# Performance work log

Hardware: AMD Instinct MI355X
Metric: run time of the kernel (lower is better)

## Reference

```python
import jax, jax.numpy as jnp
import numpy as np

# Config matching init_kwargs / module defaults
B_T2I, B_LM, B_MMU = 2, 2, 2
B = B_T2I + B_LM + B_MMU
S = 1280
H, D = 16, 64
IMAGE_BE = [(128, 1152)]          # t2i_image_begin_end
MMU_END = 1027
PAD_BE = [(0, 80), (0, 100), (0, 110), (0, 0)]  # create_block_mask default pad_begin_ends


def _mixed_mask():
    """Vectorized translation of OmniAttentionMechanism.mixed_mask -> bool [B,S,S]."""
    q = jnp.arange(S)[:, None]    # [S,1] query index
    kv = jnp.arange(S)[None, :]   # [1,S] key index

    # t2i_full_begin / t2i_full_end (per-q image block bounds)
    full_begin = jnp.arange(S)
    full_end = jnp.arange(S)
    for ib, ie in IMAGE_BE:
        full_begin = full_begin.at[ib:ie].set(ib)
        full_end = full_end.at[ib:ie].set(ie)

    # pad_ends[b, kv]: arange baseline, first len(PAD_BE) batches get pad region end
    pad_ends = jnp.tile(jnp.arange(S)[None, :], (B, 1))
    for cnt, (pb, pe) in enumerate(PAD_BE):
        pad_ends = pad_ends.at[cnt, pb:pe].set(pe)

    # t2i: padded-causal OR bidirectional image block
    causal = (~(kv < pad_ends[:, None, :]) & (q >= kv)) | (q == kv)   # [B,S,S]
    full = (kv < full_end[:, None]) & (kv >= full_begin[:, None])     # [S,S] (q-indexed bounds)
    t2i = causal | full[None]
    lm = (q >= kv)[None]                                              # [1,S,S]
    mmu = ((q >= kv) | (kv < MMU_END))[None]                          # [1,S,S]

    b = jnp.arange(B)[:, None, None]
    # Faithful to the original XOR composition (terms are batch-disjoint so == OR)
    return ((b < B_T2I) & t2i) ^ ((b >= B_T2I) & (b < B_T2I + B_LM) & lm) ^ ((b >= B_T2I + B_LM) & mmu)


def setup_inputs() -> dict:
    key = jax.random.key(0)
    kq, kk, kv = jax.random.split(key, 3)
    shape = (B, H, S, D)
    return {
        "q": jax.random.normal(kq, shape, dtype=jnp.float32),
        "k": jax.random.normal(kk, shape, dtype=jnp.float32),
        "v": jax.random.normal(kv, shape, dtype=jnp.float32),
    }


def reference(q, k, v):
    """flex_attention(q, k, v, block_mask=mixed-t2i-lm-mmu) equivalent."""
    mask = _mixed_mask()[:, None]  # [B,1,S,S], broadcast over heads
    scale = 1.0 / jnp.sqrt(jnp.float32(D))  # flex_attention default scale
    scores = jnp.einsum('bhqd,bhkd->bhqk', q, k) * scale
    scores = jnp.where(mask, scores, -jnp.inf)  # every row has >=1 allowed key (q==kv / q>=kv)
    attn = jax.nn.softmax(scores, axis=-1)
    return jnp.einsum('bhqk,bhkd->bhqd', attn, v)
```

## Files before the change

kernel.cpp:

```cpp
#include <hip/hip_runtime.h>
#include <hip/hip_bf16.h>
#include <math.h>


#define SS 1280
#define DD 64
#define NH 16
#define TK 64
#define QB 128
#define NITEMS 960

typedef __attribute__((ext_vector_type(8))) short bf16x8;
typedef __attribute__((ext_vector_type(16))) float f32x16;

union UA { uint u[4]; bf16x8 v; };

__device__ inline uint pk2(float a, float b) {
    union { __hip_bfloat162 h; uint u; } cv;
    cv.h = __float22bfloat162_rn(float2{a, b});
    return cv.u;
}

__device__ inline void pl32(uint& a, uint& b) {
    asm volatile("v_permlane32_swap_b32 %0, %1" : "+v"(a), "+v"(b));
}

#define WAITVM2() asm volatile("s_waitcnt vmcnt(2)" ::: "memory")

__device__ inline void decode_item(int i, int& b, int& h, int& qt) {
    if (i < 96)  { qt = 9; b = i / 16; h = i % 16; return; }
    i -= 96;
    if (i < 256) { b = i / 128; qt = 1 + (i % 128) / 16; h = i % 16; return; }
    i -= 256;
    if (i < 32)  { b = 2 + i / 16; qt = 8; h = i % 16; return; }
    i -= 32;
    if (i < 32)  { b = 4 + i / 16; qt = 8; h = i % 16; return; }
    i -= 32;
    if (i < 256) { b = 4 + i / 128; qt = (i % 128) / 16; h = i % 16; return; }
    i -= 256;
    if (i < 224) { qt = 7 - i / 32; b = 2 + (i % 32) / 16; h = i % 16; return; }
    i -= 224;
    if (i < 32)  { b = 2 + i / 16; qt = 0; h = i % 16; return; }
    i -= 32;
    b = i / 16; qt = 0; h = i % 16;
}

__global__ __launch_bounds__(256) void prepass8(
    const float* __restrict__ K, const float* __restrict__ V,
    ushort* __restrict__ Kb, ushort* __restrict__ Vtb)
{
    const int gx = blockIdx.x;
    const int t  = threadIdx.x;
    if (gx < 3840) {
        const size_t e = ((size_t)gx * 256 + t) * 8;
        const float4 a = *(const float4*)(K + e);
        const float4 c = *(const float4*)(K + e + 4);
        UA u;
        u.u[0] = pk2(a.x, a.y); u.u[1] = pk2(a.z, a.w);
        u.u[2] = pk2(c.x, c.y); u.u[3] = pk2(c.z, c.w);
        *(bf16x8*)(Kb + e) = u.v;
    } else {
        const int g   = gx - 3840;
        const int kvt = g % 20;
        const int p   = g / 20;
        __shared__ float T[64 * 67];
#pragma unroll
        for (int i = 0; i < 16; ++i) {
            const int idx = t + 256 * i;
            T[(idx >> 6) * 67 + (idx & 63)] = V[(size_t)p * (SS * DD) + (size_t)(kvt * 64) * DD + idx];
        }
        __syncthreads();
        ushort* dst = Vtb + (size_t)p * (DD * SS) + kvt * 64;
#pragma unroll
        for (int i = 0; i < 2; ++i) {
            const int c0 = t + 256 * i;
            const int d = c0 >> 3, kc = c0 & 7;
            UA u;
#pragma unroll
            for (int j = 0; j < 4; ++j)
                u.u[j] = pk2(T[(kc * 8 + 2 * j) * 67 + d], T[(kc * 8 + 2 * j + 1) * 67 + d]);
            *(bf16x8*)(dst + (size_t)d * SS + kc * 8) = u.v;
        }
    }
}

__global__ __launch_bounds__(256) void omni_attn15(
    const float* __restrict__ Q, const ushort* __restrict__ Kb,
    const ushort* __restrict__ Vtb, float* __restrict__ O)
{
    int b, h, qt;
    decode_item(blockIdx.x, b, h, qt);

    const int t   = threadIdx.x;
    const int w   = t >> 6;
    const int l   = t & 63;
    const int l31 = l & 31;
    const int hi2 = l >> 5;

    const int p   = b * NH + h;
    const int qb0 = qt * QB;
    const int qw0 = qb0 + w * 32;
    const int qr  = qw0 + l31;
    const size_t pbase = (size_t)p * (SS * DD);

    const int bt = (b < 2) ? 0 : (b < 4) ? 1 : 2;
    const int pe = (b == 0) ? 80 : (b == 1) ? 100 : 0;
    const int qmax_blk = qb0 + QB - 1;
    const int qmax_w   = qw0 + 31;
    const bool blk_img = (qb0 + QB - 1 >= 128) && (qb0 < 1152);
    const bool w_img   = (qw0 >= 128) && (qw0 < 1152);

    __shared__ char smem[3 * 8192];

    const float scale = 0.125f * 1.44269504088896340736f;

    int koff[2];
#pragma unroll
    for (int rd = 0; rd < 2; ++rd) {
        const int ci  = rd * 256 + w * 64 + l;
        const int row = ci >> 3, cc = ci & 7;
        koff[rd] = row * DD + (cc ^ (row & 7)) * 8;
    }

    bf16x8 qf[4];
#pragma unroll
    for (int ks = 0; ks < 4; ++ks) {
        const float* src = Q + pbase + (size_t)qr * DD + ks * 16 + hi2 * 8;
        const float4 a = *(const float4*)(src);
        const float4 c = *(const float4*)(src + 4);
        UA u;
        u.u[0] = pk2(a.x * scale, a.y * scale); u.u[1] = pk2(a.z * scale, a.w * scale);
        u.u[2] = pk2(c.x * scale, c.y * scale); u.u[3] = pk2(c.z * scale, c.w * scale);
        qf[ks] = u.v;
    }

    f32x16 o_acc[2];
#pragma unroll
    for (int ntd = 0; ntd < 2; ++ntd)
#pragma unroll
        for (int r = 0; r < 16; ++r) o_acc[ntd][r] = 0.f;
    float psum = 0.f;

    auto need_blk = [&](int k0) -> bool {
        if (bt == 0) return (k0 <= qmax_blk) || (blk_img && k0 >= 128 && k0 < 1152);
        if (bt == 1) return (k0 <= qmax_blk);
        return (k0 <= qmax_blk) || (k0 < 1027);
    };
    auto next_tile = [&](int k) -> int {
        k += TK;
        while (k < SS && !need_blk(k)) k += TK;
        return k;
    };
    auto stageK = [&](int bsel, int k0s) {
        char* buf = smem + bsel * 8192;
        const ushort* Kp = Kb + pbase + (size_t)k0s * DD;
#pragma unroll
        for (int rd = 0; rd < 2; ++rd) {
            char* lb = buf + (rd * 256 + w * 64) * 16;
            __builtin_amdgcn_global_load_lds(
                (const __attribute__((address_space(1))) void*)(Kp + koff[rd]),
                (__attribute__((address_space(3))) void*)lb, 16, 0, 0);
        }
    };

    const ushort* vrow0 = Vtb + pbase + (size_t)l31 * SS + hi2 * 8;
    const ushort* vrow1 = vrow0 + 32 * SS;

    int ka = 0, cur = 0;
    int kb = next_tile(0);
    int kc = (kb < SS) ? next_tile(kb) : SS;
    stageK(0, ka);
    stageK(1, kb);
    WAITVM2();
    __builtin_amdgcn_s_barrier();
    __builtin_amdgcn_sched_barrier(0);

    while (true) {
        const int k0 = ka;
        const bool kv_img = (k0 >= 128) && (k0 < 1152);
        bool need_w, full_w;
        if (bt == 0) {
            need_w = (k0 <= qmax_w) || (w_img && kv_img);
            full_w = ((k0 >= pe) && (k0 + 63 <= qw0)) || (w_img && kv_img);
        } else if (bt == 1) {
            need_w = (k0 <= qmax_w);
            full_w = (k0 + 63 <= qw0);
        } else {
            need_w = (k0 <= qmax_w) || (k0 < 1027);
            full_w = (k0 + 63 <= qw0) || (k0 + 63 < 1027);
        }

        if (need_w) {
            char* cbuf = smem + cur * 8192;
#pragma unroll
            for (int nt = 0; nt < 2; ++nt) {
                const int vb = k0 + nt * 32;
                bf16x8 vfn[4];
                vfn[0] = *(const bf16x8*)(vrow0 + vb);
                vfn[1] = *(const bf16x8*)(vrow0 + vb + 16);
                vfn[2] = *(const bf16x8*)(vrow1 + vb);
                vfn[3] = *(const bf16x8*)(vrow1 + vb + 16);

                f32x16 s;
#pragma unroll
                for (int r = 0; r < 16; ++r) s[r] = 0.f;
                __builtin_amdgcn_s_setprio(1);
#pragma unroll
                for (int ksd = 0; ksd < 4; ++ksd) {
                    const int row = nt * 32 + l31;
                    int off = row * 128 + ksd * 32 + hi2 * 16;
                    off ^= (row & 7) << 4;
                    const bf16x8 kf = *(const bf16x8*)(cbuf + off);
                    s = __builtin_amdgcn_mfma_f32_32x32x16_bf16(kf, qf[ksd], s, 0, 0, 0);
                }
                __builtin_amdgcn_s_setprio(0);

                const int c0k = k0 + nt * 32;
                uint c[8];
#pragma unroll
                for (int i = 0; i < 8; ++i) {
                    float pa, pb;
                    if (full_w) {
                        pa = __builtin_amdgcn_exp2f(s[2 * i]);
                        pb = __builtin_amdgcn_exp2f(s[2 * i + 1]);
                    } else {
                        const int r0i = 2 * i, r1i = 2 * i + 1;
                        const int kva = c0k + (r0i & 3) + 8 * (r0i >> 2) + 4 * hi2;
                        const int kvb = c0k + (r1i & 3) + 8 * (r1i >> 2) + 4 * hi2;
                        bool aa, ab;
                        if (bt == 0) {
                            aa = (qr == kva) | ((kva >= pe) & (qr >= kva)) |
                                 ((qr >= 128) & (qr < 1152) & (kva >= 128) & (kva < 1152));
                            ab = (qr == kvb) | ((kvb >= pe) & (qr >= kvb)) |
                                 ((qr >= 128) & (qr < 1152) & (kvb >= 128) & (kvb < 1152));
                        } else if (bt == 1) {
                            aa = (qr >= kva); ab = (qr >= kvb);
                        } else {
                            aa = (qr >= kva) | (kva < 1027);
                            ab = (qr >= kvb) | (kvb < 1027);
                        }
                        pa = aa ? __builtin_amdgcn_exp2f(s[2 * i]) : 0.f;
                        pb = ab ? __builtin_amdgcn_exp2f(s[2 * i + 1]) : 0.f;
                    }
                    psum += pa + pb;
                    c[i] = pk2(pa, pb);
                }

                UA A0, A1;
                {
                    uint a0 = c[0], b0 = c[2]; pl32(a0, b0);
                    uint a1 = c[1], b1 = c[3]; pl32(a1, b1);
                    A0.u[0] = a0; A0.u[1] = a1; A0.u[2] = b0; A0.u[3] = b1;
                    uint a2 = c[4], b2 = c[6]; pl32(a2, b2);
                    uint a3 = c[5], b3 = c[7]; pl32(a3, b3);
                    A1.u[0] = a2; A1.u[1] = a3; A1.u[2] = b2; A1.u[3] = b3;
                }

                __builtin_amdgcn_s_setprio(1);
                o_acc[0] = __builtin_amdgcn_mfma_f32_32x32x16_bf16(A0.v, vfn[0], o_acc[0], 0, 0, 0);
                o_acc[0] = __builtin_amdgcn_mfma_f32_32x32x16_bf16(A1.v, vfn[1], o_acc[0], 0, 0, 0);
                o_acc[1] = __builtin_amdgcn_mfma_f32_32x32x16_bf16(A0.v, vfn[2], o_acc[1], 0, 0, 0);
                o_acc[1] = __builtin_amdgcn_mfma_f32_32x32x16_bf16(A1.v, vfn[3], o_acc[1], 0, 0, 0);
                __builtin_amdgcn_s_setprio(0);
            }
        }

        stageK((cur + 2) % 3, (kc < SS) ? kc : 0);
        WAITVM2();
        __builtin_amdgcn_s_barrier();
        __builtin_amdgcn_sched_barrier(0);
        if (kb >= SS) break;
        ka = kb; kb = kc; kc = (kc < SS) ? next_tile(kc) : SS;
        cur = (cur + 1) % 3;
    }

    psum += __shfl_xor(psum, 32, 64);
#pragma unroll
    for (int r = 0; r < 16; ++r) {
        const int q_loc = (r & 3) + 8 * (r >> 2) + 4 * hi2;
        const float tv = __shfl(psum, q_loc, 64);
        const float iv = 1.f / tv;
        float* dst = O + pbase + (size_t)(qw0 + q_loc) * DD + l31;
#pragma unroll
        for (int ntd = 0; ntd < 2; ++ntd)
            dst[ntd * 32] = o_acc[ntd][r] * iv;
    }
}

extern "C" void kernel_launch(void* const* d_in, const int* in_sizes, int n_in,
                              void* d_out, int out_size, void* d_ws, size_t ws_size,
                              hipStream_t stream) {
    const float* q = (const float*)d_in[0];
    const float* k = (const float*)d_in[1];
    const float* v = (const float*)d_in[2];
    float* o = (float*)d_out;

    const size_t NE = 7864320ULL;
    ushort* Kb  = (ushort*)d_ws;
    ushort* Vtb = Kb + NE;

    prepass8<<<dim3(5760), 256, 0, stream>>>(k, v, Kb, Vtb);
    omni_attn15<<<dim3(NITEMS), 256, 0, stream>>>(q, Kb, Vtb, o);
}
```

Before: 100.6 us.

## Load K fragments directly from global memory, drop LDS staging pipeline

Replaces the triple-buffered LDS staging of K tiles (global_load_lds plus per-tile barriers) with direct per-wave global loads of K fragments into registers. Tile skipping becomes per-wave instead of per-block, so waves iterate independently without workgroup synchronisation. This removes barrier stalls and LDS traffic, but gives up explicit prefetch and makes the four waves each fetch the same K rows from cache, which may expose global load latency.

```diff
diff --git a/kernel.cpp b/kernel.cpp
--- a/kernel.cpp
+++ b/kernel.cpp
@@ -24,8 +24,6 @@
 __device__ inline void pl32(uint& a, uint& b) {
     asm volatile("v_permlane32_swap_b32 %0, %1" : "+v"(a), "+v"(b));
 }
-
-#define WAITVM2() asm volatile("s_waitcnt vmcnt(2)" ::: "memory")
 
 __device__ inline void decode_item(int i, int& b, int& h, int& qt) {
     if (i < 96)  { qt = 9; b = i / 16; h = i % 16; return; }
@@ -84,7 +82,7 @@
     }
 }
 
-__global__ __launch_bounds__(256) void omni_attn15(
+__global__ __launch_bounds__(256) void omni_attn16(
     const float* __restrict__ Q, const ushort* __restrict__ Kb,
     const ushort* __restrict__ Vtb, float* __restrict__ O)
 {
@@ -105,22 +103,10 @@
 
     const int bt = (b < 2) ? 0 : (b < 4) ? 1 : 2;
     const int pe = (b == 0) ? 80 : (b == 1) ? 100 : 0;
-    const int qmax_blk = qb0 + QB - 1;
-    const int qmax_w   = qw0 + 31;
-    const bool blk_img = (qb0 + QB - 1 >= 128) && (qb0 < 1152);
-    const bool w_img   = (qw0 >= 128) && (qw0 < 1152);
-
-    __shared__ char smem[3 * 8192];
+    const int qmax_w = qw0 + 31;
+    const bool w_img = (qw0 >= 128) && (qw0 < 1152);
 
     const float scale = 0.125f * 1.44269504088896340736f;
-
-    int koff[2];
-#pragma unroll
-    for (int rd = 0; rd < 2; ++rd) {
-        const int ci  = rd * 256 + w * 64 + l;
-        const int row = ci >> 3, cc = ci & 7;
-        koff[rd] = row * DD + (cc ^ (row & 7)) * 8;
-    }
 
     bf16x8 qf[4];
 #pragma unroll
@@ -141,137 +127,97 @@
         for (int r = 0; r < 16; ++r) o_acc[ntd][r] = 0.f;
     float psum = 0.f;
 
-    auto need_blk = [&](int k0) -> bool {
-        if (bt == 0) return (k0 <= qmax_blk) || (blk_img && k0 >= 128 && k0 < 1152);
-        if (bt == 1) return (k0 <= qmax_blk);
-        return (k0 <= qmax_blk) || (k0 < 1027);
+    const ushort* kfb = Kb + pbase + (size_t)l31 * DD + hi2 * 8;
+    const ushort* vr0 = Vtb + pbase + (size_t)l31 * SS + hi2 * 8;
+    const ushort* vr1 = vr0 + 32 * SS;
+
+    auto need_w_f = [&](int k0) -> bool {
+        if (bt == 0) return (k0 <= qmax_w) || (w_img && k0 >= 128 && k0 < 1152);
+        if (bt == 1) return (k0 <= qmax_w);
+        return (k0 <= qmax_w) || (k0 < 1027);
     };
-    auto next_tile = [&](int k) -> int {
-        k += TK;
-        while (k < SS && !need_blk(k)) k += TK;
-        return k;
-    };
-    auto stageK = [&](int bsel, int k0s) {
-        char* buf = smem + bsel * 8192;
-        const ushort* Kp = Kb + pbase + (size_t)k0s * DD;
-#pragma unroll
-        for (int rd = 0; rd < 2; ++rd) {
-            char* lb = buf + (rd * 256 + w * 64) * 16;
-            __builtin_amdgcn_global_load_lds(
-                (const __attribute__((address_space(1))) void*)(Kp + koff[rd]),
-                (__attribute__((address_space(3))) void*)lb, 16, 0, 0);
+
+    int k0 = 0;
+    while (k0 < SS) {
+        bool full_w;
+        if (bt == 0)      full_w = ((k0 >= pe) && (k0 + 63 <= qw0)) || (w_img && k0 >= 128 && k0 < 1152);
+        else if (bt == 1) full_w = (k0 + 63 <= qw0);
+        else              full_w = (k0 + 63 <= qw0) || (k0 + 63 < 1027);
+
+#pragma unroll
+        for (int nt = 0; nt < 2; ++nt) {
+            const int kvb_ = k0 + nt * 32;
+
+            const ushort* kp = kfb + (size_t)kvb_ * DD;
+            const bf16x8 kf0 = *(const bf16x8*)(kp);
+            const bf16x8 kf1 = *(const bf16x8*)(kp + 16);
+            const bf16x8 kf2 = *(const bf16x8*)(kp + 32);
+            const bf16x8 kf3 = *(const bf16x8*)(kp + 48);
+            const bf16x8 vf0 = *(const bf16x8*)(vr0 + kvb_);
+            const bf16x8 vf1 = *(const bf16x8*)(vr0 + kvb_ + 16);
+            const bf16x8 vf2 = *(const bf16x8*)(vr1 + kvb_);
+            const bf16x8 vf3 = *(const bf16x8*)(vr1 + kvb_ + 16);
+
+            f32x16 s;
+#pragma unroll
+            for (int r = 0; r < 16; ++r) s[r] = 0.f;
+            __builtin_amdgcn_s_setprio(1);
+            s = __builtin_amdgcn_mfma_f32_32x32x16_bf16(kf0, qf[0], s, 0, 0, 0);
+            s = __builtin_amdgcn_mfma_f32_32x32x16_bf16(kf1, qf[1], s, 0, 0, 0);
+            s = __builtin_amdgcn_mfma_f32_32x32x16_bf16(kf2, qf[2], s, 0, 0, 0);
+            s = __builtin_amdgcn_mfma_f32_32x32x16_bf16(kf3, qf[3], s, 0, 0, 0);
+            __builtin_amdgcn_s_setprio(0);
+
+            uint c[8];
+#pragma unroll
+            for (int i = 0; i < 8; ++i) {
+                float pa, pb;
+                if (full_w) {
+                    pa = __builtin_amdgcn_exp2f(s[2 * i]);
+                    pb = __builtin_amdgcn_exp2f(s[2 * i + 1]);
+                } else {
+                    const int r0i = 2 * i, r1i = 2 * i + 1;
+                    const int kva = kvb_ + (r0i & 3) + 8 * (r0i >> 2) + 4 * hi2;
+                    const int kvb2 = kvb_ + (r1i & 3) + 8 * (r1i >> 2) + 4 * hi2;
+                    bool aa, ab;
+                    if (bt == 0) {
+                        aa = (qr == kva) | ((kva >= pe) & (qr >= kva)) |
+                             ((qr >= 128) & (qr < 1152) & (kva >= 128) & (kva < 1152));
+                        ab = (qr == kvb2) | ((kvb2 >= pe) & (qr >= kvb2)) |
+                             ((qr >= 128) & (qr < 1152) & (kvb2 >= 128) & (kvb2 < 1152));
+                    } else if (bt == 1) {
+                        aa = (qr >= kva); ab = (qr >= kvb2);
+                    } else {
+                        aa = (qr >= kva) | (kva < 1027);
+                        ab = (qr >= kvb2) | (kvb2 < 1027);
+                    }
+                    pa = aa ? __builtin_amdgcn_exp2f(s[2 * i]) : 0.f;
+                    pb = ab ? __builtin_amdgcn_exp2f(s[2 * i + 1]) : 0.f;
+                }
+                psum += pa + pb;
+                c[i] = pk2(pa, pb);
+            }
+
+            UA A0, A1;
+            {
+                uint a0 = c[0], b0 = c[2]; pl32(a0, b0);
+                uint a1 = c[1], b1 = c[3]; pl32(a1, b1);
+                A0.u[0] = a0; A0.u[1] = a1; A0.u[2] = b0; A0.u[3] = b1;
+                uint a2 = c[4], b2 = c[6]; pl32(a2, b2);
+                uint a3 = c[5], b3 = c[7]; pl32(a3, b3);
+                A1.u[0] = a2; A1.u[1] = a3; A1.u[2] = b2; A1.u[3] = b3;
+            }
+
+            __builtin_amdgcn_s_setprio(1);
+            o_acc[0] = __builtin_amdgcn_mfma_f32_32x32x16_bf16(A0.v, vf0, o_acc[0], 0, 0, 0);
+            o_acc[0] = __builtin_amdgcn_mfma_f32_32x32x16_bf16(A1.v, vf1, o_acc[0], 0, 0, 0);
+            o_acc[1] = __builtin_amdgcn_mfma_f32_32x32x16_bf16(A0.v, vf2, o_acc[1], 0, 0, 0);
+            o_acc[1] = __builtin_amdgcn_mfma_f32_32x32x16_bf16(A1.v, vf3, o_acc[1], 0, 0, 0);
+            __builtin_amdgcn_s_setprio(0);
         }
-    };
-
-    const ushort* vrow0 = Vtb + pbase + (size_t)l31 * SS + hi2 * 8;
-    const ushort* vrow1 = vrow0 + 32 * SS;
-
-    int ka = 0, cur = 0;
-    int kb = next_tile(0);
-    int kc = (kb < SS) ? next_tile(kb) : SS;
-    stageK(0, ka);
-    stageK(1, kb);
-    WAITVM2();
-    __builtin_amdgcn_s_barrier();
-    __builtin_amdgcn_sched_barrier(0);
-
-    while (true) {
-        const int k0 = ka;
-        const bool kv_img = (k0 >= 128) && (k0 < 1152);
-        bool need_w, full_w;
-        if (bt == 0) {
-            need_w = (k0 <= qmax_w) || (w_img && kv_img);
-            full_w = ((k0 >= pe) && (k0 + 63 <= qw0)) || (w_img && kv_img);
-        } else if (bt == 1) {
-            need_w = (k0 <= qmax_w);
-            full_w = (k0 + 63 <= qw0);
-        } else {
-            need_w = (k0 <= qmax_w) || (k0 < 1027);
-            full_w = (k0 + 63 <= qw0) || (k0 + 63 < 1027);
-        }
-
-        if (need_w) {
-            char* cbuf = smem + cur * 8192;
-#pragma unroll
-            for (int nt = 0; nt < 2; ++nt) {
-                const int vb = k0 + nt * 32;
-                bf16x8 vfn[4];
-                vfn[0] = *(const bf16x8*)(vrow0 + vb);
-                vfn[1] = *(const bf16x8*)(vrow0 + vb + 16);
-                vfn[2] = *(const bf16x8*)(vrow1 + vb);
-                vfn[3] = *(const bf16x8*)(vrow1 + vb + 16);
-
-                f32x16 s;
-#pragma unroll
-                for (int r = 0; r < 16; ++r) s[r] = 0.f;
-                __builtin_amdgcn_s_setprio(1);
-#pragma unroll
-                for (int ksd = 0; ksd < 4; ++ksd) {
-                    const int row = nt * 32 + l31;
-                    int off = row * 128 + ksd * 32 + hi2 * 16;
-                    off ^= (row & 7) << 4;
-                    const bf16x8 kf = *(const bf16x8*)(cbuf + off);
-                    s = __builtin_amdgcn_mfma_f32_32x32x16_bf16(kf, qf[ksd], s, 0, 0, 0);
-                }
-                __builtin_amdgcn_s_setprio(0);
-
-                const int c0k = k0 + nt * 32;
-                uint c[8];
-#pragma unroll
-                for (int i = 0; i < 8; ++i) {
-                    float pa, pb;
-                    if (full_w) {
-                        pa = __builtin_amdgcn_exp2f(s[2 * i]);
-                        pb = __builtin_amdgcn_exp2f(s[2 * i + 1]);
-                    } else {
-                        const int r0i = 2 * i, r1i = 2 * i + 1;
-                        const int kva = c0k + (r0i & 3) + 8 * (r0i >> 2) + 4 * hi2;
-                        const int kvb = c0k + (r1i & 3) + 8 * (r1i >> 2) + 4 * hi2;
-                        bool aa, ab;
-                        if (bt == 0) {
-                            aa = (qr == kva) | ((kva >= pe) & (qr >= kva)) |
-                                 ((qr >= 128) & (qr < 1152) & (kva >= 128) & (kva < 1152));
-                            ab = (qr == kvb) | ((kvb >= pe) & (qr >= kvb)) |
-                                 ((qr >= 128) & (qr < 1152) & (kvb >= 128) & (kvb < 1152));
-                        } else if (bt == 1) {
-                            aa = (qr >= kva); ab = (qr >= kvb);
-                        } else {
-                            aa = (qr >= kva) | (kva < 1027);
-                            ab = (qr >= kvb) | (kvb < 1027);
-                        }
-                        pa = aa ? __builtin_amdgcn_exp2f(s[2 * i]) : 0.f;
-                        pb = ab ? __builtin_amdgcn_exp2f(s[2 * i + 1]) : 0.f;
-                    }
-                    psum += pa + pb;
-                    c[i] = pk2(pa, pb);
-                }
-
-                UA A0, A1;
-                {
-                    uint a0 = c[0], b0 = c[2]; pl32(a0, b0);
-                    uint a1 = c[1], b1 = c[3]; pl32(a1, b1);
-                    A0.u[0] = a0; A0.u[1] = a1; A0.u[2] = b0; A0.u[3] = b1;
-                    uint a2 = c[4], b2 = c[6]; pl32(a2, b2);
-                    uint a3 = c[5], b3 = c[7]; pl32(a3, b3);
-                    A1.u[0] = a2; A1.u[1] = a3; A1.u[2] = b2; A1.u[3] = b3;
-                }
-
-                __builtin_amdgcn_s_setprio(1);
-                o_acc[0] = __builtin_amdgcn_mfma_f32_32x32x16_bf16(A0.v, vfn[0], o_acc[0], 0, 0, 0);
-                o_acc[0] = __builtin_amdgcn_mfma_f32_32x32x16_bf16(A1.v, vfn[1], o_acc[0], 0, 0, 0);
-                o_acc[1] = __builtin_amdgcn_mfma_f32_32x32x16_bf16(A0.v, vfn[2], o_acc[1], 0, 0, 0);
-                o_acc[1] = __builtin_amdgcn_mfma_f32_32x32x16_bf16(A1.v, vfn[3], o_acc[1], 0, 0, 0);
-                __builtin_amdgcn_s_setprio(0);
-            }
-        }
-
-        stageK((cur + 2) % 3, (kc < SS) ? kc : 0);
-        WAITVM2();
-        __builtin_amdgcn_s_barrier();
-        __builtin_amdgcn_sched_barrier(0);
-        if (kb >= SS) break;
-        ka = kb; kb = kc; kc = (kc < SS) ? next_tile(kc) : SS;
-        cur = (cur + 1) % 3;
+
+        k0 += TK;
+        while (k0 < SS && !need_w_f(k0)) k0 += TK;
     }
 
     psum += __shfl_xor(psum, 32, 64);
@@ -300,5 +246,5 @@
     ushort* Vtb = Kb + NE;
 
     prepass8<<<dim3(5760), 256, 0, stream>>>(k, v, Kb, Vtb);
-    omni_attn15<<<dim3(NITEMS), 256, 0, stream>>>(q, Kb, Vtb, o);
-}
+    omni_attn16<<<dim3(NITEMS), 256, 0, stream>>>(q, Kb, Vtb, o);
+}
```

Measured after the change: 139.2 us. 1.38x slower.
